# Optimization experiments

Hardware: AMD Instinct MI355X
Metric: run time of the kernel (lower is better)

The kernel has to match this reference:

```python
import jax, jax.numpy as jnp
import numpy as np
from jax import lax

N, D, H = 4096, 256, 4


def setup_inputs() -> dict:
    key = jax.random.key(0)
    ks = jax.random.split(key, 6)
    x = jax.random.normal(ks[0], (1, 1, N, D), dtype=jnp.float32)
    adj = jax.random.randint(ks[1], (N, N), 0, 2, dtype=jnp.int32)
    conv_w = jax.random.normal(ks[2], (1, 1, 1, 1), dtype=jnp.float32)
    conv_b = jax.random.normal(ks[3], (1,), dtype=jnp.float32)
    # xavier_uniform on (H, 2D, 1) with gain 1.414
    limit = 1.414 * np.sqrt(6.0 / (2 * D + 1))
    a = jax.random.uniform(ks[4], (H, 2 * D, 1), minval=-limit, maxval=limit, dtype=jnp.float32)
    bias = jnp.zeros((D,), dtype=jnp.float32)
    return {"x": x, "adj": adj, "conv_w": conv_w, "conv_b": conv_b, "a": a, "bias": bias}


def reference(x, adj, conv_w, conv_b, a, bias):
    # 1x1 conv (NCHW / OIHW), preserves spatial dims
    h = lax.conv_general_dilated(x, conv_w, (1, 1), 'VALID',
                                 dimension_numbers=('NCHW', 'OIHW', 'NCHW'))
    h = h + conv_b[None, :, None, None]
    h = h[0, 0]                      # [N, D]
    d = h.shape[1]
    a1 = a[:, :d, 0]                 # [H, D]
    a2 = a[:, d:, 0]                 # [H, D]
    Wh1 = h @ a1.T                   # [N, H]
    Wh2 = h @ a2.T                   # [N, H]
    # e[k, i, j] = elu(Wh1[i, k] + Wh2[j, k])
    e = jax.nn.elu(Wh1.T[:, :, None] + Wh2.T[:, None, :])   # [H, N, N]
    att = jnp.where((adj > 0)[None, :, :], e, jnp.float32(-9e15))
    att = jax.nn.softmax(att, axis=-1)
    # dropout is inactive in eval mode (self.training=False)
    h_pass = jnp.einsum('hij,jd->hid', att, h).mean(axis=0)  # [N, D]
    out = jax.nn.elu(0.5 * h_pass + 0.5 * h)
    norm = jnp.maximum(jnp.linalg.norm(out, axis=1, keepdims=True), 1e-12)
    out = out / norm
    return out + bias
```

## Files before the change

kernel.cpp:

```cpp
#include <hip/hip_runtime.h>
#include <math.h>

#define NN 4096
#define DD 256
#define HH 4
#define SPLIT 4
#define BKG 64

typedef short short8 __attribute__((ext_vector_type(8)));
typedef float float4v __attribute__((ext_vector_type(4)));

__device__ __forceinline__ unsigned short f2bf(float f) {
  unsigned u = __float_as_uint(f);
  u += 0x7FFF + ((u >> 16) & 1);
  return (unsigned short)(u >> 16);
}
__device__ __forceinline__ unsigned f2bf_pk(float a, float b) {
  unsigned ua = __float_as_uint(a); ua += 0x7FFF + ((ua >> 16) & 1);
  unsigned ub = __float_as_uint(b); ub += 0x7FFF + ((ub >> 16) & 1);
  return __builtin_amdgcn_perm(ub, ua, 0x07060302);
}
__device__ __forceinline__ void gld16(void* lds, const void* gp) {
  __builtin_amdgcn_global_load_lds(
      (const __attribute__((address_space(1))) unsigned int*)gp,
      (__attribute__((address_space(3))) unsigned int*)lds, 16, 0, 0);
}

__global__ void k_zero(float* __restrict__ hp) {
  int idx = blockIdx.x * 256 + threadIdx.x;
  ((float4*)hp)[idx] = make_float4(0.f, 0.f, 0.f, 0.f);
}

__global__ __launch_bounds__(256) void k_pre(
    const float* __restrict__ x, const float* __restrict__ a,
    const float* __restrict__ cwp, const float* __restrict__ cbp,
    unsigned short* __restrict__ hbfT, float* __restrict__ Rpg,
    unsigned short* __restrict__ Ebf) {
  const int tid = threadIdx.x;
  const int bid = blockIdx.x;
  const float cw = cwp[0], cb = cbp[0];

  if (bid < 256) {
    __shared__ float t[64][65];
    const int j0 = (bid & 63) * 64, d0 = (bid >> 6) * 64;
    const int r = tid >> 4, c4 = tid & 15;
#pragma unroll
    for (int p = 0; p < 4; p++) {
      const int jj = p * 16 + r;
      const float4 v = *(const float4*)(x + (size_t)(j0 + jj) * DD + d0 + c4 * 4);
      t[jj][c4 * 4 + 0] = v.x * cw + cb;
      t[jj][c4 * 4 + 1] = v.y * cw + cb;
      t[jj][c4 * 4 + 2] = v.z * cw + cb;
      t[jj][c4 * 4 + 3] = v.w * cw + cb;
    }
    __syncthreads();
    const int jc = (tid & 15) * 4, db = tid >> 4;
#pragma unroll
    for (int p = 0; p < 4; p++) {
      const int dd = p * 16 + db;
      const unsigned l0 = f2bf(t[jc + 0][dd]);
      const unsigned l1 = f2bf(t[jc + 1][dd]);
      const unsigned l2 = f2bf(t[jc + 2][dd]);
      const unsigned l3 = f2bf(t[jc + 3][dd]);
      uint2 val;
      val.x = l0 | (l1 << 16);
      val.y = l2 | (l3 << 16);
      *(uint2*)(hbfT + (size_t)(d0 + dd) * NN + j0 + jc) = val;
    }
  } else {
    const int ln = tid >> 2, qd = (tid & 3) * 64;
    const int node = (bid - 256) * 64 + ln;
    float p1[HH] = {0.f, 0.f, 0.f, 0.f}, p2[HH] = {0.f, 0.f, 0.f, 0.f};
#pragma unroll
    for (int k = 0; k < 16; k++) {
      const int d = qd + k * 4;
      const float4 v = *(const float4*)(x + (size_t)node * DD + d);
      const float h0 = v.x * cw + cb, h1 = v.y * cw + cb;
      const float h2 = v.z * cw + cb, h3 = v.w * cw + cb;
#pragma unroll
      for (int h = 0; h < HH; h++) {
        const float4 a1 = *(const float4*)(a + h * 512 + d);
        const float4 a2 = *(const float4*)(a + h * 512 + 256 + d);
        p1[h] += h0 * a1.x + h1 * a1.y + h2 * a1.z + h3 * a1.w;
        p2[h] += h0 * a2.x + h1 * a2.y + h2 * a2.z + h3 * a2.w;
      }
    }
#pragma unroll
    for (int off = 1; off <= 2; off <<= 1) {
#pragma unroll
      for (int h = 0; h < HH; h++) {
        p1[h] += __shfl_xor(p1[h], off);
        p2[h] += __shfl_xor(p2[h], off);
      }
    }
    if ((tid & 3) == 0) {
#pragma unroll
      for (int h = 0; h < HH; h++) {
        Rpg[h * NN + node] = __expf(p1[h]);
        Ebf[h * NN + node] = f2bf(__expf(p2[h]));
      }
    }
  }
}

__global__ __launch_bounds__(256) void k_zw(
    const int* __restrict__ adj, const float* __restrict__ Rpg,
    const unsigned short* __restrict__ Ebf, unsigned short* __restrict__ Wm) {
  __shared__ float red[4][HH];
  __shared__ float sZi[HH];

  const int i = blockIdx.x;
  const int tid = threadIdx.x;
  const float C = 0.36787944117144233f;
  float Rp[HH], z[HH];
#pragma unroll
  for (int h = 0; h < HH; h++) {
    Rp[h] = Rpg[h * NN + i];
    z[h] = 0.f;
  }
  float P[4][HH][4];
  const int4* arow = (const int4*)(adj + (size_t)i * NN);
#pragma unroll
  for (int k = 0; k < 4; k++) {
    const int j4 = tid + k * 256;
    const int4 av = arow[j4];
    const bool m0 = av.x > 0, m1 = av.y > 0, m2 = av.z > 0, m3 = av.w > 0;
#pragma unroll
    for (int h = 0; h < HH; h++) {
      const uint2 e2 = *(const uint2*)(Ebf + (size_t)h * NN + j4 * 4);
      const float E0 = __uint_as_float(e2.x << 16);
      const float E1 = __uint_as_float(e2.x & 0xffff0000u);
      const float E2 = __uint_as_float(e2.y << 16);
      const float E3 = __uint_as_float(e2.y & 0xffff0000u);
      float u, p0, p1, p2, p3;
      u = Rp[h] * E0; p0 = u > 1.f ? u : C * __expf(u); p0 = m0 ? p0 : 0.f;
      u = Rp[h] * E1; p1 = u > 1.f ? u : C * __expf(u); p1 = m1 ? p1 : 0.f;
      u = Rp[h] * E2; p2 = u > 1.f ? u : C * __expf(u); p2 = m2 ? p2 : 0.f;
      u = Rp[h] * E3; p3 = u > 1.f ? u : C * __expf(u); p3 = m3 ? p3 : 0.f;
      z[h] += (p0 + p1) + (p2 + p3);
      P[k][h][0] = p0; P[k][h][1] = p1; P[k][h][2] = p2; P[k][h][3] = p3;
    }
  }
#pragma unroll
  for (int h = 0; h < HH; h++) {
#pragma unroll
    for (int off = 32; off; off >>= 1) z[h] += __shfl_xor(z[h], off);
  }
  const int lane = tid & 63, wv = tid >> 6;
  if (lane == 0) {
#pragma unroll
    for (int h = 0; h < HH; h++) red[wv][h] = z[h];
  }
  __syncthreads();
  if (tid < HH) {
    const float zt = red[0][tid] + red[1][tid] + red[2][tid] + red[3][tid];
    sZi[tid] = zt > 0.f ? 0.25f / zt : 0.f;
  }
  __syncthreads();
  float Zi[HH];
#pragma unroll
  for (int h = 0; h < HH; h++) Zi[h] = sZi[h];

  unsigned* wrow = (unsigned*)(Wm + (size_t)i * NN);
#pragma unroll
  for (int k = 0; k < 4; k++) {
    const int j4 = tid + k * 256;
    float w0 = 0.f, w1 = 0.f, w2 = 0.f, w3 = 0.f;
#pragma unroll
    for (int h = 0; h < HH; h++) {
      w0 += P[k][h][0] * Zi[h];
      w1 += P[k][h][1] * Zi[h];
      w2 += P[k][h][2] * Zi[h];
      w3 += P[k][h][3] * Zi[h];
    }
    wrow[j4 * 2] = f2bf_pk(w0, w1);
    wrow[j4 * 2 + 1] = f2bf_pk(w2, w3);
  }
}

__global__ __launch_bounds__(256) void k_gemm(
    const unsigned short* __restrict__ Wm, const unsigned short* __restrict__ hbfT,
    float* __restrict__ hpOut, int useSplit) {
  extern __shared__ __align__(16) unsigned short smem[];
  unsigned short* sA0 = smem;
  unsigned short* sA1 = smem + 4096;
  unsigned short* sB0 = smem + 8192;
  unsigned short* sB1 = smem + 8192 + 16384;
  const int tid = threadIdx.x;
  const int wv = tid >> 6, lane = tid & 63;
  const int m16 = lane & 15, q = lane >> 4, m7 = m16 & 7;
  const int rb = blockIdx.x >> 2, sp = blockIdx.x & 3;
  const int i0 = rb * 64;
  const int jlo = sp * (NN / SPLIT);
  const int lr = lane >> 3;
  const int lk8 = (lane & 7) ^ lr;
  const int NT = (NN / SPLIT) / BKG;

  float4v acc[4][4];
#pragma unroll
  for (int a = 0; a < 4; a++)
#pragma unroll
    for (int b = 0; b < 4; b++) acc[a][b] = (float4v)0.f;

  {
    const int j0 = jlo;
#pragma unroll
    for (int t = 0; t < 2; t++) {
      const int r0 = wv * 16 + t * 8;
      gld16(sA0 + r0 * 64, Wm + (size_t)(i0 + r0 + lr) * NN + j0 + lk8 * 8);
    }
#pragma unroll
    for (int t = 0; t < 8; t++) {
      const int r0 = wv * 64 + t * 8;
      gld16(sB0 + r0 * 64, hbfT + (size_t)(r0 + lr) * NN + j0 + lk8 * 8);
    }
  }

  for (int kt = 0; kt < NT; kt++) {
    const unsigned short* sAb = (kt & 1) ? sA1 : sA0;
    const unsigned short* sBb = (kt & 1) ? sB1 : sB0;
    unsigned short* sAn = (kt & 1) ? sA0 : sA1;
    unsigned short* sBn = (kt & 1) ? sB0 : sB1;

    if (kt + 1 < NT) {
      const int j0 = jlo + (kt + 1) * BKG;
#pragma unroll
      for (int t = 0; t < 2; t++) {
        const int r0 = wv * 16 + t * 8;
        gld16(sAn + r0 * 64, Wm + (size_t)(i0 + r0 + lr) * NN + j0 + lk8 * 8);
      }
#pragma unroll
      for (int t = 0; t < 8; t++) {
        const int r0 = wv * 64 + t * 8;
        gld16(sBn + r0 * 64, hbfT + (size_t)(r0 + lr) * NN + j0 + lk8 * 8);
      }
      asm volatile("s_waitcnt vmcnt(10)" ::: "memory");
    } else {
      asm volatile("s_waitcnt vmcnt(0)" ::: "memory");
    }
    __builtin_amdgcn_s_barrier();
    __builtin_amdgcn_sched_barrier(0);

#pragma unroll
    for (int ks = 0; ks < 2; ks++) {
      const int kp = ((ks * 4 + q) ^ m7) * 8;
      short8 aF[4], bF[4];
#pragma unroll
      for (int it = 0; it < 4; it++)
        aF[it] = *(const short8*)(sAb + (it * 16 + m16) * 64 + kp);
#pragma unroll
      for (int dt = 0; dt < 4; dt++)
        bF[dt] = *(const short8*)(sBb + (wv * 64 + dt * 16 + m16) * 64 + kp);
#pragma unroll
      for (int it = 0; it < 4; it++)
#pragma unroll
        for (int dt = 0; dt < 4; dt++)
          acc[it][dt] = __builtin_amdgcn_mfma_f32_16x16x32_bf16(aF[it], bF[dt], acc[it][dt], 0, 0, 0);
    }
    __builtin_amdgcn_sched_barrier(0);
    __builtin_amdgcn_s_barrier();
  }

  if (useSplit) {
    float* base = hpOut + (size_t)sp * NN * DD;
#pragma unroll
    for (int it = 0; it < 4; it++)
#pragma unroll
      for (int dt = 0; dt < 4; dt++) {
        const int d = wv * 64 + dt * 16 + m16;
#pragma unroll
        for (int rg = 0; rg < 4; rg++)
          base[(size_t)(i0 + it * 16 + q * 4 + rg) * DD + d] = acc[it][dt][rg];
      }
  } else {
#pragma unroll
    for (int it = 0; it < 4; it++)
#pragma unroll
      for (int dt = 0; dt < 4; dt++) {
        const int d = wv * 64 + dt * 16 + m16;
#pragma unroll
        for (int rg = 0; rg < 4; rg++)
          atomicAdd(&hpOut[(size_t)(i0 + it * 16 + q * 4 + rg) * DD + d], acc[it][dt][rg]);
      }
  }
}

__global__ __launch_bounds__(256) void k_epi(
    const float* __restrict__ hp, int nsplit, const float* __restrict__ x,
    const float* __restrict__ cwp, const float* __restrict__ cbp,
    const float* __restrict__ bias, float* __restrict__ out) {
  const int lane = threadIdx.x & 63, wv = threadIdx.x >> 6;
  const int i = blockIdx.x * 4 + wv;
  const float cw = cwp[0], cb = cbp[0];
  const int d4 = lane * 4;
  float4 pv = make_float4(0.f, 0.f, 0.f, 0.f);
  for (int s = 0; s < nsplit; s++) {
    const float4 t = *(const float4*)(hp + (size_t)s * NN * DD + (size_t)i * DD + d4);
    pv.x += t.x; pv.y += t.y; pv.z += t.z; pv.w += t.w;
  }
  const float4 xv = *(const float4*)(x + (size_t)i * DD + d4);
  float4 v;
  v.x = 0.5f * pv.x + 0.5f * (xv.x * cw + cb);
  v.y = 0.5f * pv.y + 0.5f * (xv.y * cw + cb);
  v.z = 0.5f * pv.z + 0.5f * (xv.z * cw + cb);
  v.w = 0.5f * pv.w + 0.5f * (xv.w * cw + cb);
  v.x = v.x > 0.f ? v.x : expm1f(v.x);
  v.y = v.y > 0.f ? v.y : expm1f(v.y);
  v.z = v.z > 0.f ? v.z : expm1f(v.z);
  v.w = v.w > 0.f ? v.w : expm1f(v.w);
  float ss = v.x * v.x + v.y * v.y + v.z * v.z + v.w * v.w;
#pragma unroll
  for (int off = 32; off; off >>= 1) ss += __shfl_xor(ss, off);
  const float inv = 1.f / fmaxf(sqrtf(ss), 1e-12f);
  const float4 bv = *(const float4*)(bias + d4);
  float4 o;
  o.x = v.x * inv + bv.x;
  o.y = v.y * inv + bv.y;
  o.z = v.z * inv + bv.z;
  o.w = v.w * inv + bv.w;
  *(float4*)(out + (size_t)i * DD + d4) = o;
}

extern "C" void kernel_launch(void* const* d_in, const int* in_sizes, int n_in,
                              void* d_out, int out_size, void* d_ws, size_t ws_size,
                              hipStream_t stream) {
  const float* x = (const float*)d_in[0];
  const int* adj = (const int*)d_in[1];
  const float* cw = (const float*)d_in[2];
  const float* cb = (const float*)d_in[3];
  const float* a = (const float*)d_in[4];
  const float* bias = (const float*)d_in[5];
  float* out = (float*)d_out;
  float* ws = (float*)d_ws;

  float* Rpg = ws;
  unsigned short* Ebf = (unsigned short*)(ws + 16384);
  unsigned short* hbfT = (unsigned short*)(ws + 24576);
  unsigned short* Wm = (unsigned short*)(ws + 24576 + 524288);
  float* hp = ws + 24576 + 524288 + 8388608;

  const size_t needSplit =
      (size_t)(24576 + 524288 + 8388608 + (size_t)SPLIT * NN * DD) * 4;
  const int useSplit = (ws_size >= needSplit) ? 1 : 0;
  const int nsplit = useSplit ? SPLIT : 1;

  static int smemDone = 0;
  if (!smemDone) {
    (void)hipFuncSetAttribute((const void*)k_gemm,
                              hipFuncAttributeMaxDynamicSharedMemorySize, 81920);
    smemDone = 1;
  }

  if (!useSplit) hipLaunchKernelGGL(k_zero, dim3(NN * DD / 1024), dim3(256), 0, stream, hp);
  hipLaunchKernelGGL(k_pre, dim3(320), dim3(256), 0, stream, x, a, cw, cb, hbfT, Rpg, Ebf);
  hipLaunchKernelGGL(k_zw, dim3(NN), dim3(256), 0, stream, adj, Rpg, Ebf, Wm);
  hipLaunchKernelGGL(k_gemm, dim3(64 * SPLIT), dim3(256), 81920, stream, Wm, hbfT, hp, useSplit);
  hipLaunchKernelGGL(k_epi, dim3(1024), dim3(256), 0, stream, hp, nsplit, x, cw, cb, bias, out);
}
```

Baseline: 162.2 us.

## Fuse epilogue into split-K GEMM via last-block counter and raise split to 8

Raises the split-K factor from 4 to 8, giving 512 GEMM blocks instead of 256 so more CUs have work. It also removes the separate epilogue launch: each row-block keeps an atomic counter, zeroed in k_zw, and the last split block to finish sums the partials and applies ELU, L2 normalisation and bias. This saves a kernel launch and lets the epilogue overlap with other GEMM blocks. In exchange it writes and re-reads twice as much partial-sum memory, adds threadfence and atomic overhead, and runs the tail epilogue on only 64 blocks.

```diff
diff --git a/kernel.cpp b/kernel.cpp
--- a/kernel.cpp
+++ b/kernel.cpp
@@ -4,7 +4,7 @@
 #define NN 4096
 #define DD 256
 #define HH 4
-#define SPLIT 4
+#define SPLIT 8
 #define BKG 64
 
 typedef short short8 __attribute__((ext_vector_type(8)));
@@ -105,12 +105,14 @@
 
 __global__ __launch_bounds__(256) void k_zw(
     const int* __restrict__ adj, const float* __restrict__ Rpg,
-    const unsigned short* __restrict__ Ebf, unsigned short* __restrict__ Wm) {
+    const unsigned short* __restrict__ Ebf, unsigned short* __restrict__ Wm,
+    int* __restrict__ cnt) {
   __shared__ float red[4][HH];
   __shared__ float sZi[HH];
 
   const int i = blockIdx.x;
   const int tid = threadIdx.x;
+  if (i == 0 && tid < 64) cnt[tid] = 0;
   const float C = 0.36787944117144233f;
   float Rp[HH], z[HH];
 #pragma unroll
@@ -180,7 +182,10 @@
 
 __global__ __launch_bounds__(256) void k_gemm(
     const unsigned short* __restrict__ Wm, const unsigned short* __restrict__ hbfT,
-    float* __restrict__ hpOut, int useSplit) {
+    float* __restrict__ hpOut, int useSplit, int* __restrict__ cnt,
+    const float* __restrict__ x, const float* __restrict__ cwp,
+    const float* __restrict__ cbp, const float* __restrict__ bias,
+    float* __restrict__ outp) {
   extern __shared__ __align__(16) unsigned short smem[];
   unsigned short* sA0 = smem;
   unsigned short* sA1 = smem + 4096;
@@ -189,7 +194,7 @@
   const int tid = threadIdx.x;
   const int wv = tid >> 6, lane = tid & 63;
   const int m16 = lane & 15, q = lane >> 4, m7 = m16 & 7;
-  const int rb = blockIdx.x >> 2, sp = blockIdx.x & 3;
+  const int rb = blockIdx.x >> 3, sp = blockIdx.x & 7;
   const int i0 = rb * 64;
   const int jlo = sp * (NN / SPLIT);
   const int lr = lane >> 3;
@@ -272,6 +277,48 @@
         for (int rg = 0; rg < 4; rg++)
           base[(size_t)(i0 + it * 16 + q * 4 + rg) * DD + d] = acc[it][dt][rg];
       }
+
+    __threadfence();
+    __shared__ int sLast;
+    if (tid == 0) sLast = (atomicAdd(&cnt[rb], 1) == SPLIT - 1);
+    __syncthreads();
+    if (!sLast) return;
+    __threadfence();
+
+    const float cw = cwp[0], cb = cbp[0];
+    const int row0 = i0 + wv * 16;
+    const int d4 = lane * 4;
+#pragma unroll 2
+    for (int r = 0; r < 16; r++) {
+      const int i = row0 + r;
+      float4 pv = make_float4(0.f, 0.f, 0.f, 0.f);
+#pragma unroll
+      for (int s = 0; s < SPLIT; s++) {
+        const float4 t = *(const float4*)(hpOut + (size_t)s * NN * DD + (size_t)i * DD + d4);
+        pv.x += t.x; pv.y += t.y; pv.z += t.z; pv.w += t.w;
+      }
+      const float4 xv = *(const float4*)(x + (size_t)i * DD + d4);
+      float4 v;
+      v.x = 0.5f * pv.x + 0.5f * (xv.x * cw + cb);
+      v.y = 0.5f * pv.y + 0.5f * (xv.y * cw + cb);
+      v.z = 0.5f * pv.z + 0.5f * (xv.z * cw + cb);
+      v.w = 0.5f * pv.w + 0.5f * (xv.w * cw + cb);
+      v.x = v.x > 0.f ? v.x : expm1f(v.x);
+      v.y = v.y > 0.f ? v.y : expm1f(v.y);
+      v.z = v.z > 0.f ? v.z : expm1f(v.z);
+      v.w = v.w > 0.f ? v.w : expm1f(v.w);
+      float ss = v.x * v.x + v.y * v.y + v.z * v.z + v.w * v.w;
+#pragma unroll
+      for (int off = 32; off; off >>= 1) ss += __shfl_xor(ss, off);
+      const float inv = 1.f / fmaxf(sqrtf(ss), 1e-12f);
+      const float4 bv = *(const float4*)(bias + d4);
+      float4 o;
+      o.x = v.x * inv + bv.x;
+      o.y = v.y * inv + bv.y;
+      o.z = v.z * inv + bv.z;
+      o.w = v.w * inv + bv.w;
+      *(float4*)(outp + (size_t)i * DD + d4) = o;
+    }
   } else {
 #pragma unroll
     for (int it = 0; it < 4; it++)
@@ -338,9 +385,10 @@
   unsigned short* hbfT = (unsigned short*)(ws + 24576);
   unsigned short* Wm = (unsigned short*)(ws + 24576 + 524288);
   float* hp = ws + 24576 + 524288 + 8388608;
+  int* cnt = (int*)(ws + 24576 + 524288 + 8388608 + (size_t)SPLIT * NN * DD);
 
   const size_t needSplit =
-      (size_t)(24576 + 524288 + 8388608 + (size_t)SPLIT * NN * DD) * 4;
+      (size_t)(24576 + 524288 + 8388608 + (size_t)SPLIT * NN * DD + 64) * 4;
   const int useSplit = (ws_size >= needSplit) ? 1 : 0;
   const int nsplit = useSplit ? SPLIT : 1;
 
@@ -353,7 +401,9 @@
 
   if (!useSplit) hipLaunchKernelGGL(k_zero, dim3(NN * DD / 1024), dim3(256), 0, stream, hp);
   hipLaunchKernelGGL(k_pre, dim3(320), dim3(256), 0, stream, x, a, cw, cb, hbfT, Rpg, Ebf);
-  hipLaunchKernelGGL(k_zw, dim3(NN), dim3(256), 0, stream, adj, Rpg, Ebf, Wm);
-  hipLaunchKernelGGL(k_gemm, dim3(64 * SPLIT), dim3(256), 81920, stream, Wm, hbfT, hp, useSplit);
-  hipLaunchKernelGGL(k_epi, dim3(1024), dim3(256), 0, stream, hp, nsplit, x, cw, cb, bias, out);
-}
+  hipLaunchKernelGGL(k_zw, dim3(NN), dim3(256), 0, stream, adj, Rpg, Ebf, Wm, cnt);
+  hipLaunchKernelGGL(k_gemm, dim3(64 * SPLIT), dim3(256), 81920, stream,
+                     Wm, hbfT, hp, useSplit, cnt, x, cw, cb, bias, out);
+  if (!useSplit)
+    hipLaunchKernelGGL(k_epi, dim3(1024), dim3(256), 0, stream, hp, nsplit, x, cw, cb, bias, out);
+}
```

Result: slower. 281.9 us (+73.8%).
